# Kernel optimization log

Measured on AMD Instinct MI355X. Metric: run time of the kernel, lower is better.

Reference implementation:

```python
import jax, jax.numpy as jnp
import numpy as np

N = 100000      # nodes
E = 1600000     # edges (before self loops)
IN_DIM, EMB, HID, OUT, L = 128, 128, 128, 64, 3
LN_EPS = 1e-5


def _lin(k, fi, fo):
    return (jax.random.normal(k, (fi, fo), jnp.float32) / np.sqrt(fi)).astype(jnp.float32)


def setup_inputs() -> dict:
    key = jax.random.key(0)
    ks = jax.random.split(key, 8)
    x = jax.random.normal(ks[0], (N, IN_DIM), jnp.float32)
    edge_index = jax.random.randint(ks[1], (2, E), 0, N, dtype=jnp.int64)
    # in-degree of destination nodes (as data.degree would provide)
    degree = jnp.zeros((N,), jnp.float32).at[edge_index[1]].add(1.0)
    lks = jax.random.split(ks[2], 2 * L)
    W1 = jnp.stack([_lin(lks[2 * i], EMB, HID) for i in range(L)])
    W2 = jnp.stack([_lin(lks[2 * i + 1], HID, EMB) for i in range(L)])
    return dict(
        x=x, edge_index=edge_index, degree=degree,
        Win=_lin(ks[3], IN_DIM, EMB), b_in=jnp.zeros((EMB,), jnp.float32),
        W1=W1, b1=jnp.zeros((L, HID), jnp.float32),
        W2=W2, b2=jnp.zeros((L, EMB), jnp.float32),
        ln_g=jnp.ones((L, EMB), jnp.float32), ln_b=jnp.zeros((L, EMB), jnp.float32),
        out_g=jnp.ones((EMB,), jnp.float32), out_b=jnp.zeros((EMB,), jnp.float32),
        Wout=_lin(ks[4], EMB, OUT), b_out=jnp.zeros((OUT,), jnp.float32),
    )


def _layernorm(h, g, b):
    m = h.mean(-1, keepdims=True)
    v = ((h - m) ** 2).mean(-1, keepdims=True)
    return (h - m) * jax.lax.rsqrt(v + LN_EPS) * g + b


def reference(x, edge_index, degree, Win, b_in, W1, b1, W2, b2,
              ln_g, ln_b, out_g, out_b, Wout, b_out):
    # input_lin: Linear -> Dropout(eval: identity) -> ReLU
    h = jax.nn.relu(x @ Win + b_in)                        # [N, EMB]
    # add self loops, degree + 1
    loop = jnp.arange(N, dtype=edge_index.dtype)
    src = jnp.concatenate([edge_index[0], loop])           # [E+N]
    dst = jnp.concatenate([edge_index[1], loop])
    inv = jax.lax.rsqrt(degree + 1.0)                      # deg^{-1/2}
    coef = (inv[src] * inv[dst])[:, None]                  # symmetric GCN norm
    for i in range(L):
        m = h @ W1[i] + b1[i]                              # [N, HID]
        agg = jax.ops.segment_sum(m[src] * coef, dst, num_segments=N)  # gather-scatter
        out = agg @ W2[i] + b2[i]                          # [N, EMB]
        h = jax.nn.relu(_layernorm(out + h, ln_g[i], ln_b[i]))  # residual + LN + act (dropout=id)
    h = _layernorm(h, out_g, out_b)
    return h @ Wout + b_out
```

## Files before the change

kernel.cpp:

```cpp
#include <hip/hip_runtime.h>
#include <cstdint>
#include <cstddef>

typedef unsigned short u16;
typedef unsigned int u32;
typedef __attribute__((ext_vector_type(2))) unsigned short u16x2;
typedef __attribute__((ext_vector_type(4))) unsigned short u16x4;
typedef __attribute__((ext_vector_type(8))) unsigned short u16x8;
typedef __attribute__((ext_vector_type(8))) __bf16 bf16x8;
typedef __attribute__((ext_vector_type(4))) float f32x4;

#define PREP_F32   0
#define PREP_BF16  1
#define PREP_LN    2
#define EPI_IN    0
#define EPI_SCALE 1
#define EPI_NONE  3

__device__ __forceinline__ float wred(float v) {
#pragma unroll
  for (int m = 32; m >= 1; m >>= 1) v += __shfl_xor(v, m, 64);
  return v;
}
__device__ __forceinline__ u16 f2bf(float f) {
  u32 u = __float_as_uint(f);
  u += 0x7fffu + ((u >> 16) & 1u);
  return (u16)(u >> 16);
}
__device__ __forceinline__ float bflo(u32 u) { return __uint_as_float(u << 16); }
__device__ __forceinline__ float bfhi(u32 u) { return __uint_as_float(u & 0xffff0000u); }
__device__ __forceinline__ u32 pack2(float a, float b) {
  u32 ua = __float_as_uint(a); ua += 0x7fffu + ((ua >> 16) & 1u);
  u32 ub = __float_as_uint(b); ub += 0x7fffu + ((ub >> 16) & 1u);
  return (ua >> 16) | (ub & 0xffff0000u);
}

__global__ void scan_block_k(const float* __restrict__ deg, int* __restrict__ offs,
                             int* __restrict__ bsum, int N) {
  __shared__ int sh[256];
  int tid = threadIdx.x;
  int i = blockIdx.x * 256 + tid;
  int c = (i < N) ? (int)(deg[i] + 0.5f) : 0;
  int val = c;
  for (int off = 1; off < 256; off <<= 1) {
    sh[tid] = val; __syncthreads();
    if (tid >= off) val += sh[tid - off];
    __syncthreads();
  }
  if (i < N) offs[i] = val - c;
  if (tid == 255) bsum[blockIdx.x] = val;
}

__global__ void scan_bsum_k(int* __restrict__ bsum, int nb) {
  __shared__ int sh[1024];
  int tid = threadIdx.x;
  int c = (tid < nb) ? bsum[tid] : 0;
  int val = c;
  for (int off = 1; off < 1024; off <<= 1) {
    sh[tid] = val; __syncthreads();
    if (tid >= off) val += sh[tid - off];
    __syncthreads();
  }
  if (tid < nb) bsum[tid] = val - c;
}

__global__ void scan_add_k(int* __restrict__ offs, const int* __restrict__ bsum,
                           int* __restrict__ gcur, float* __restrict__ inv,
                           const float* __restrict__ deg, int N, int E) {
  int i = blockIdx.x * 256 + threadIdx.x;
  if (i < N) {
    int o = offs[i] + bsum[i >> 8];
    offs[i] = o;
    inv[i] = rsqrtf(deg[i] + 1.0f);
    if ((i & 511) == 0) gcur[i >> 9] = o;
  } else if (i == N) {
    offs[N] = E;
  }
}

__global__ __launch_bounds__(256) void scatter_k(
    const int* __restrict__ src, const int* __restrict__ dst,
    int* __restrict__ gcur, uint2* __restrict__ pairs, int E) {
  __shared__ int hist[256];
  __shared__ int base_[256];
  const int tid = threadIdx.x;
  const int e0 = blockIdx.x * 8192;
  const int e1 = min(E, e0 + 8192);
  hist[tid] = 0;
  __syncthreads();
  for (int e = e0 + tid; e < e1; e += 256)
    atomicAdd(&hist[dst[e] >> 9], 1);
  __syncthreads();
  int c = hist[tid];
  if (c > 0) base_[tid] = atomicAdd(&gcur[tid], c);
  hist[tid] = 0;
  __syncthreads();
  for (int e = e0 + tid; e < e1; e += 256) {
    int d = dst[e];
    int b = d >> 9;
    int r = atomicAdd(&hist[b], 1);
    pairs[base_[b] + r] = make_uint2((u32)src[e], (u32)d);
  }
}

__global__ __launch_bounds__(256) void fill2_k(
    const uint2* __restrict__ pairs, const int* __restrict__ offs,
    int* __restrict__ col, int N) {
  __shared__ int cur[512];
  const int b = blockIdx.x;
  const int n0 = b << 9;
  const int n1 = min(N, n0 + 512);
  const int tid = threadIdx.x;
  for (int i = tid; i < n1 - n0; i += 256) cur[i] = offs[n0 + i];
  __syncthreads();
  const int e0 = offs[n0], e1 = offs[n1];
  for (int e = e0 + tid; e < e1; e += 256) {
    uint2 pr = pairs[e];
    int p = atomicAdd(&cur[(int)pr.y - n0], 1);
    col[p] = (int)pr.x;
  }
}

__global__ void pack_all_k(const float* __restrict__ Win, const float* __restrict__ W1,
                           const float* __restrict__ W2, const float* __restrict__ Wout,
                           u16* __restrict__ pWin, u16* __restrict__ pW1,
                           u16* __restrict__ pW2, u16* __restrict__ pWout) {
  const int b = blockIdx.x;
  const float* W; u16* P; int ncol; int t;
  if (b < 8)       { W = Win;                        P = pWin;                      ncol = 128; t = b * 256 + threadIdx.x; }
  else if (b < 32) { int l = (b - 8) / 8;  W = W1 + (size_t)l * 16384;  P = pW1 + (size_t)l * 16384; ncol = 128; t = ((b - 8) % 8) * 256 + threadIdx.x; }
  else if (b < 56) { int l = (b - 32) / 8; W = W2 + (size_t)l * 16384;  P = pW2 + (size_t)l * 16384; ncol = 128; t = ((b - 32) % 8) * 256 + threadIdx.x; }
  else             { W = Wout;                       P = pWout;                     ncol = 64;  t = (b - 56) * 256 + threadIdx.x; }
  int NT = ncol >> 4;
  int total = 4 * NT * 64;
  if (t >= total) return;
  int lane = t & 63;
  int tmp = t >> 6;
  int nt = tmp % NT, kc = tmp / NT;
  int n = nt * 16 + (lane & 15);
  int kb = kc * 32 + ((lane >> 4) << 2);
  u16* dst = P + (size_t)t * 8;
#pragma unroll
  for (int j = 0; j < 8; ++j) {
    int k = kb + (j & 3) + ((j >> 2) << 4);
    dst[j] = f2bf(W[(size_t)k * ncol + n]);
  }
}

__global__ __launch_bounds__(256) void spmm_gemm_k(
    const uint4* __restrict__ msc, const int* __restrict__ offs,
    const int* __restrict__ col, const float* __restrict__ inv,
    const u16* __restrict__ Wp, const float* __restrict__ bias,
    u32* __restrict__ h, const float* __restrict__ g1,
    const float* __restrict__ lb1, int N) {
  __shared__ union {
    u16  xs[32][136];
    float cs[32][132];
  } sh;
  const int tid = threadIdx.x;
  const int lane = tid & 63, wid = tid >> 6;
  const int row0 = blockIdx.x * 32;
  const int g = lane >> 4, c = lane & 15;

  for (int rr = 0; rr < 8; ++rr) {
    const int d = row0 + wid * 8 + rr;
    const int s0 = offs[d], s1 = offs[d + 1];
    float2 a0 = {0.f, 0.f}, a1 = {0.f, 0.f}, a2 = {0.f, 0.f}, a3 = {0.f, 0.f};
    int base = s0;
    const int nfull = s0 + ((s1 - s0) & ~15);
    for (; base < nfull; base += 16) {
      int sA = col[base + g];
      int sB = col[base + 4 + g];
      int sC = col[base + 8 + g];
      int sD = col[base + 12 + g];
      uint4 rA = msc[(size_t)sA * 16 + c];
      uint4 rB = msc[(size_t)sB * 16 + c];
      uint4 rC = msc[(size_t)sC * 16 + c];
      uint4 rD = msc[(size_t)sD * 16 + c];
      a0.x += bflo(rA.x); a0.y += bfhi(rA.x);
      a1.x += bflo(rA.y); a1.y += bfhi(rA.y);
      a2.x += bflo(rA.z); a2.y += bfhi(rA.z);
      a3.x += bflo(rA.w); a3.y += bfhi(rA.w);
      a0.x += bflo(rB.x); a0.y += bfhi(rB.x);
      a1.x += bflo(rB.y); a1.y += bfhi(rB.y);
      a2.x += bflo(rB.z); a2.y += bfhi(rB.z);
      a3.x += bflo(rB.w); a3.y += bfhi(rB.w);
      a0.x += bflo(rC.x); a0.y += bfhi(rC.x);
      a1.x += bflo(rC.y); a1.y += bfhi(rC.y);
      a2.x += bflo(rC.z); a2.y += bfhi(rC.z);
      a3.x += bflo(rC.w); a3.y += bfhi(rC.w);
      a0.x += bflo(rD.x); a0.y += bfhi(rD.x);
      a1.x += bflo(rD.y); a1.y += bfhi(rD.y);
      a2.x += bflo(rD.z); a2.y += bfhi(rD.z);
      a3.x += bflo(rD.w); a3.y += bfhi(rD.w);
    }
    if (base < s1) {
      const int last = s1 - 1;
      int jA = base + g, jB = base + 4 + g, jC = base + 8 + g, jD = base + 12 + g;
      int sA = col[min(jA, last)];
      int sB = col[min(jB, last)];
      int sC = col[min(jC, last)];
      int sD = col[min(jD, last)];
      uint4 rA = msc[(size_t)sA * 16 + c];
      uint4 rB = msc[(size_t)sB * 16 + c];
      uint4 rC = msc[(size_t)sC * 16 + c];
      uint4 rD = msc[(size_t)sD * 16 + c];
      float mA = (jA <= last) ? 1.f : 0.f;
      float mB = (jB <= last) ? 1.f : 0.f;
      float mC = (jC <= last) ? 1.f : 0.f;
      float mD = (jD <= last) ? 1.f : 0.f;
      a0.x = fmaf(mA, bflo(rA.x), a0.x); a0.y = fmaf(mA, bfhi(rA.x), a0.y);
      a1.x = fmaf(mA, bflo(rA.y), a1.x); a1.y = fmaf(mA, bfhi(rA.y), a1.y);
      a2.x = fmaf(mA, bflo(rA.z), a2.x); a2.y = fmaf(mA, bfhi(rA.z), a2.y);
      a3.x = fmaf(mA, bflo(rA.w), a3.x); a3.y = fmaf(mA, bfhi(rA.w), a3.y);
      a0.x = fmaf(mB, bflo(rB.x), a0.x); a0.y = fmaf(mB, bfhi(rB.x), a0.y);
      a1.x = fmaf(mB, bflo(rB.y), a1.x); a1.y = fmaf(mB, bfhi(rB.y), a1.y);
      a2.x = fmaf(mB, bflo(rB.z), a2.x); a2.y = fmaf(mB, bfhi(rB.z), a2.y);
      a3.x = fmaf(mB, bflo(rB.w), a3.x); a3.y = fmaf(mB, bfhi(rB.w), a3.y);
      a0.x = fmaf(mC, bflo(rC.x), a0.x); a0.y = fmaf(mC, bfhi(rC.x), a0.y);
      a1.x = fmaf(mC, bflo(rC.y), a1.x); a1.y = fmaf(mC, bfhi(rC.y), a1.y);
      a2.x = fmaf(mC, bflo(rC.z), a2.x); a2.y = fmaf(mC, bfhi(rC.z), a2.y);
      a3.x = fmaf(mC, bflo(rC.w), a3.x); a3.y = fmaf(mC, bfhi(rC.w), a3.y);
      a0.x = fmaf(mD, bflo(rD.x), a0.x); a0.y = fmaf(mD, bfhi(rD.x), a0.y);
      a1.x = fmaf(mD, bflo(rD.y), a1.x); a1.y = fmaf(mD, bfhi(rD.y), a1.y);
      a2.x = fmaf(mD, bflo(rD.z), a2.x); a2.y = fmaf(mD, bfhi(rD.z), a2.y);
      a3.x = fmaf(mD, bflo(rD.w), a3.x); a3.y = fmaf(mD, bfhi(rD.w), a3.y);
    }
    a0.x += __shfl_xor(a0.x, 16, 64); a0.x += __shfl_xor(a0.x, 32, 64);
    a0.y += __shfl_xor(a0.y, 16, 64); a0.y += __shfl_xor(a0.y, 32, 64);
    a1.x += __shfl_xor(a1.x, 16, 64); a1.x += __shfl_xor(a1.x, 32, 64);
    a1.y += __shfl_xor(a1.y, 16, 64); a1.y += __shfl_xor(a1.y, 32, 64);
    a2.x += __shfl_xor(a2.x, 16, 64); a2.x += __shfl_xor(a2.x, 32, 64);
    a2.y += __shfl_xor(a2.y, 16, 64); a2.y += __shfl_xor(a2.y, 32, 64);
    a3.x += __shfl_xor(a3.x, 16, 64); a3.x += __shfl_xor(a3.x, 32, 64);
    a3.y += __shfl_xor(a3.y, 16, 64); a3.y += __shfl_xor(a3.y, 32, 64);
    if (g == 0) {
      uint4 r = msc[(size_t)d * 16 + c];
      float iv = inv[d];
      uint4 o;
      o.x = pack2((a0.x + bflo(r.x)) * iv, (a0.y + bfhi(r.x)) * iv);
      o.y = pack2((a1.x + bflo(r.y)) * iv, (a1.y + bfhi(r.y)) * iv);
      o.z = pack2((a2.x + bflo(r.z)) * iv, (a2.y + bfhi(r.z)) * iv);
      o.w = pack2((a3.x + bflo(r.w)) * iv, (a3.y + bfhi(r.w)) * iv);
      *(uint4*)&sh.xs[wid * 8 + rr][c * 8] = o;
    }
  }
  __syncthreads();

  const int m0  = (wid >> 1) << 4;
  const int ntb = (wid & 1) << 2;
  f32x4 acc[4];
#pragma unroll
  for (int t = 0; t < 4; ++t) acc[t] = (f32x4){0.f, 0.f, 0.f, 0.f};
  const int ar  = m0 + (lane & 15);
  const int akb = (lane >> 4) << 2;
  const bf16x8* Bp = (const bf16x8*)Wp;
#pragma unroll
  for (int kc = 0; kc < 4; ++kc) {
    u16x4 lo = *(const u16x4*)&sh.xs[ar][kc * 32 + akb];
    u16x4 hi = *(const u16x4*)&sh.xs[ar][kc * 32 + akb + 16];
    u16x8 av;
#pragma unroll
    for (int j = 0; j < 4; ++j) { av[j] = lo[j]; av[j + 4] = hi[j]; }
    bf16x8 a = __builtin_bit_cast(bf16x8, av);
#pragma unroll
    for (int t = 0; t < 4; ++t) {
      bf16x8 b = Bp[(kc * 8 + ntb + t) * 64 + lane];
      acc[t] = __builtin_amdgcn_mfma_f32_16x16x32_bf16(a, b, acc[t], 0, 0, 0);
    }
  }

  const int cb = lane & 15;
  const int rg = (lane >> 4) << 2;
  __syncthreads();
#pragma unroll
  for (int t = 0; t < 4; ++t) {
    int colm = (ntb + t) * 16 + cb;
    float bv = bias[colm];
#pragma unroll
    for (int r = 0; r < 4; ++r) sh.cs[m0 + rg + r][colm] = acc[t][r] + bv;
  }
  __syncthreads();
  float2 gg = *(const float2*)&g1[lane * 2];
  float2 bb = *(const float2*)&lb1[lane * 2];
  for (int rr = 0; rr < 8; ++rr) {
    int r = wid * 8 + rr;
    int gr = row0 + r;
    float2 t2 = *(const float2*)&sh.cs[r][lane * 2];
    u32 hv = h[(size_t)gr * 64 + lane];
    float tx = t2.x + bflo(hv), ty = t2.y + bfhi(hv);
    float mean = wred(tx + ty) * (1.f / 128.f);
    float dx = tx - mean, dy = ty - mean;
    float var = wred(dx * dx + dy * dy) * (1.f / 128.f);
    float rstd = rsqrtf(var + 1e-5f);
    float y0 = fmaxf(dx * rstd * gg.x + bb.x, 0.f);
    float y1 = fmaxf(dy * rstd * gg.y + bb.y, 0.f);
    h[(size_t)gr * 64 + lane] = pack2(y0, y1);
  }
}

template <int NOUT, int PREP, int EPI>
__global__ __launch_bounds__(256) void gemm_mfma(
    const void* __restrict__ Xv, const u16* __restrict__ Wp,
    const float* __restrict__ bias, void* __restrict__ Yv,
    const void* __restrict__ resv,
    const float* __restrict__ g1, const float* __restrict__ lb1,
    int N) {
  constexpr int NT = NOUT / 16;
  __shared__ union {
    u16  xs[32][136];
    float cs[32][132];
  } sh;
  const int tid = threadIdx.x;
  const int lane = tid & 63, wid = tid >> 6;
  const int row0 = blockIdx.x * 32;

  if constexpr (PREP == PREP_F32) {
    const float* X = (const float*)Xv;
    for (int i = tid; i < 1024; i += 256) {
      int r = i >> 5, c4 = i & 31;
      float4 v = ((const float4*)(X + (size_t)(row0 + r) * 128))[c4];
      u16x4 o = {f2bf(v.x), f2bf(v.y), f2bf(v.z), f2bf(v.w)};
      *(u16x4*)&sh.xs[r][c4 * 4] = o;
    }
  } else if constexpr (PREP == PREP_BF16) {
    const u16x4* X = (const u16x4*)Xv;
    for (int i = tid; i < 1024; i += 256) {
      int r = i >> 5, c4 = i & 31;
      *(u16x4*)&sh.xs[r][c4 * 4] = X[(size_t)(row0 + r) * 32 + c4];
    }
  } else {
    const u32* X = (const u32*)Xv;
    float2 gg = *(const float2*)&g1[lane * 2];
    float2 bb = *(const float2*)&lb1[lane * 2];
    for (int rr = 0; rr < 8; ++rr) {
      int r = wid * 8 + rr;
      u32 v = X[(size_t)(row0 + r) * 64 + lane];
      float tx = bflo(v), ty = bfhi(v);
      float mean = wred(tx + ty) * (1.f / 128.f);
      float dx = tx - mean, dy = ty - mean;
      float var = wred(dx * dx + dy * dy) * (1.f / 128.f);
      float rstd = rsqrtf(var + 1e-5f);
      u16x2 o = {f2bf(dx * rstd * gg.x + bb.x), f2bf(dy * rstd * gg.y + bb.y)};
      *(u16x2*)&sh.xs[r][lane * 2] = o;
    }
  }
  __syncthreads();

  constexpr int NTW = (NOUT == 128) ? 4 : 2;
  const int m0  = (NOUT == 128) ? ((wid >> 1) << 4) : ((wid & 1) << 4);
  const int ntb = (NOUT == 128) ? ((wid & 1) << 2) : ((wid >> 1) << 1);

  f32x4 acc[NTW];
#pragma unroll
  for (int t = 0; t < NTW; ++t) acc[t] = (f32x4){0.f, 0.f, 0.f, 0.f};

  const int ar  = m0 + (lane & 15);
  const int akb = (lane >> 4) << 2;
  const bf16x8* Bp = (const bf16x8*)Wp;
#pragma unroll
  for (int kc = 0; kc < 4; ++kc) {
    u16x4 lo = *(const u16x4*)&sh.xs[ar][kc * 32 + akb];
    u16x4 hi = *(const u16x4*)&sh.xs[ar][kc * 32 + akb + 16];
    u16x8 av;
#pragma unroll
    for (int j = 0; j < 4; ++j) { av[j] = lo[j]; av[j + 4] = hi[j]; }
    bf16x8 a = __builtin_bit_cast(bf16x8, av);
#pragma unroll
    for (int t = 0; t < NTW; ++t) {
      bf16x8 b = Bp[(kc * NT + ntb + t) * 64 + lane];
      acc[t] = __builtin_amdgcn_mfma_f32_16x16x32_bf16(a, b, acc[t], 0, 0, 0);
    }
  }

  const int cb = lane & 15;
  const int rg = (lane >> 4) << 2;
  if constexpr (EPI == EPI_NONE) {
    float* Y = (float*)Yv;
#pragma unroll
    for (int t = 0; t < NTW; ++t) {
      int col = (ntb + t) * 16 + cb;
      float bv = bias[col];
#pragma unroll
      for (int r = 0; r < 4; ++r) {
        int gr = row0 + m0 + rg + r;
        Y[(size_t)gr * NOUT + col] = acc[t][r] + bv;
      }
    }
  } else if constexpr (EPI == EPI_SCALE) {
    const float* inv = (const float*)resv;
    u16* Y = (u16*)Yv;
#pragma unroll
    for (int t = 0; t < NTW; ++t) {
      int col = (ntb + t) * 16 + cb;
      float bv = bias[col];
#pragma unroll
      for (int r = 0; r < 4; ++r) {
        int gr = row0 + m0 + rg + r;
        Y[(size_t)gr * NOUT + col] = f2bf((acc[t][r] + bv) * inv[gr]);
      }
    }
  } else {
    __syncthreads();
#pragma unroll
    for (int t = 0; t < NTW; ++t) {
      int col = (ntb + t) * 16 + cb;
      float bv = bias[col];
#pragma unroll
      for (int r = 0; r < 4; ++r) sh.cs[m0 + rg + r][col] = acc[t][r] + bv;
    }
    __syncthreads();
    u32* Y = (u32*)Yv;
    for (int rr = 0; rr < 8; ++rr) {
      int r = wid * 8 + rr;
      int gr = row0 + r;
      float2 t2 = *(const float2*)&sh.cs[r][lane * 2];
      Y[(size_t)gr * 64 + lane] = pack2(fmaxf(t2.x, 0.f), fmaxf(t2.y, 0.f));
    }
  }
}

extern "C" void kernel_launch(void* const* d_in, const int* in_sizes, int n_in,
                              void* d_out, int out_size, void* d_ws, size_t ws_size,
                              hipStream_t stream) {
  (void)n_in; (void)out_size; (void)ws_size;
  const float* x      = (const float*)d_in[0];
  const int*   eidx   = (const int*)d_in[1];
  const float* degree = (const float*)d_in[2];
  const float* Win    = (const float*)d_in[3];
  const float* b_in   = (const float*)d_in[4];
  const float* W1     = (const float*)d_in[5];
  const float* b1     = (const float*)d_in[6];
  const float* W2     = (const float*)d_in[7];
  const float* b2     = (const float*)d_in[8];
  const float* ln_g   = (const float*)d_in[9];
  const float* ln_b   = (const float*)d_in[10];
  const float* out_g  = (const float*)d_in[11];
  const float* out_b  = (const float*)d_in[12];
  const float* Wout   = (const float*)d_in[13];
  const float* b_out  = (const float*)d_in[14];

  const int N = in_sizes[0] / 128;
  const int E = in_sizes[1] / 2;
  const int* esrc = eidx;
  const int* edst = eidx + E;

  char* p = (char*)d_ws;
  auto alloc = [&](size_t bytes) {
    char* q = p;
    p += (bytes + 255) & ~(size_t)255;
    return q;
  };
  float* inv    = (float*)alloc((size_t)N * 4);
  int*   offs   = (int*)alloc(((size_t)N + 1) * 4);
  int*   gcur   = (int*)alloc(256 * 4);
  int*   bsum   = (int*)alloc(1024 * 4);
  int*   col    = (int*)alloc((size_t)E * 4);
  uint2* pairs  = (uint2*)alloc((size_t)E * 8);
  u32*   h      = (u32*)alloc((size_t)N * 128 * 2);
  u32*   msc    = (u32*)alloc((size_t)N * 128 * 2);
  u16*   pWin   = (u16*)alloc(4 * 8 * 64 * 8 * 2);
  u16*   pWout  = (u16*)alloc(4 * 4 * 64 * 8 * 2);
  u16*   pW1    = (u16*)alloc(3 * 4 * 8 * 64 * 8 * 2);
  u16*   pW2    = (u16*)alloc(3 * 4 * 8 * 64 * 8 * 2);

  pack_all_k<<<60, 256, 0, stream>>>(Win, W1, W2, Wout, pWin, pW1, pW2, pWout);

  const int nb = (N + 255) / 256;
  const int NB = (N + 511) / 512;
  scan_block_k<<<nb, 256, 0, stream>>>(degree, offs, bsum, N);
  scan_bsum_k<<<1, 1024, 0, stream>>>(bsum, nb);
  scan_add_k<<<(N + 256) / 256, 256, 0, stream>>>(offs, bsum, gcur, inv, degree, N, E);
  scatter_k<<<(E + 8191) / 8192, 256, 0, stream>>>(esrc, edst, gcur, pairs, E);
  fill2_k<<<NB, 256, 0, stream>>>(pairs, offs, col, N);

  const int gemmGrid = (N + 31) / 32;

  gemm_mfma<128, PREP_F32, EPI_IN><<<gemmGrid, 256, 0, stream>>>(
      x, pWin, b_in, h, nullptr, nullptr, nullptr, N);
  for (int l = 0; l < 3; ++l) {
    gemm_mfma<128, PREP_BF16, EPI_SCALE><<<gemmGrid, 256, 0, stream>>>(
        h, pW1 + (size_t)l * 16384, b1 + l * 128, msc, inv, nullptr, nullptr, N);
    spmm_gemm_k<<<gemmGrid, 256, 0, stream>>>(
        (const uint4*)msc, offs, col, inv, pW2 + (size_t)l * 16384,
        b2 + l * 128, h, ln_g + l * 128, ln_b + l * 128, N);
  }
  gemm_mfma<64, PREP_LN, EPI_NONE><<<gemmGrid, 256, 0, stream>>>(
      h, pWout, b_out, d_out, nullptr, out_g, out_b, N);
}
```

Baseline: 391.3 us.

## Pack edge pairs into 32 bits and map one row per quarter-wave in SpMM

The bucketed scatter now stores each edge as a single 32-bit word, holding the 17-bit source and the 9-bit local destination, which halves the pairs buffer traffic. In the fused SpMM+GEMM kernel each 16-lane group now owns its own destination row instead of the whole wave splitting one row's edges and reducing with cross-lane shuffles, which removes the shuffle reduction. Each group walks its neighbour list serially in steps of four with masking. The LayerNorm epilogue is split into two 16-row halves so the shared float buffer shrinks, at the cost of extra barriers. Packing assumes N < 131072, and per-row work imbalance within a wave may rise.

```diff
diff --git a/kernel.cpp b/kernel.cpp
--- a/kernel.cpp
+++ b/kernel.cpp
@@ -80,7 +80,7 @@
 
 __global__ __launch_bounds__(256) void scatter_k(
     const int* __restrict__ src, const int* __restrict__ dst,
-    int* __restrict__ gcur, uint2* __restrict__ pairs, int E) {
+    int* __restrict__ gcur, u32* __restrict__ pairs, int E) {
   __shared__ int hist[256];
   __shared__ int base_[256];
   const int tid = threadIdx.x;
@@ -99,12 +99,12 @@
     int d = dst[e];
     int b = d >> 9;
     int r = atomicAdd(&hist[b], 1);
-    pairs[base_[b] + r] = make_uint2((u32)src[e], (u32)d);
+    pairs[base_[b] + r] = (u32)src[e] | ((u32)(d & 511) << 17);
   }
 }
 
 __global__ __launch_bounds__(256) void fill2_k(
-    const uint2* __restrict__ pairs, const int* __restrict__ offs,
+    const u32* __restrict__ pairs, const int* __restrict__ offs,
     int* __restrict__ col, int N) {
   __shared__ int cur[512];
   const int b = blockIdx.x;
@@ -115,9 +115,9 @@
   __syncthreads();
   const int e0 = offs[n0], e1 = offs[n1];
   for (int e = e0 + tid; e < e1; e += 256) {
-    uint2 pr = pairs[e];
-    int p = atomicAdd(&cur[(int)pr.y - n0], 1);
-    col[p] = (int)pr.x;
+    u32 pr = pairs[e];
+    int p = atomicAdd(&cur[pr >> 17], 1);
+    col[p] = (int)(pr & 0x1FFFFu);
   }
 }
 
@@ -155,64 +155,36 @@
     const float* __restrict__ lb1, int N) {
   __shared__ union {
     u16  xs[32][136];
-    float cs[32][132];
+    float cs[16][132];
   } sh;
   const int tid = threadIdx.x;
   const int lane = tid & 63, wid = tid >> 6;
   const int row0 = blockIdx.x * 32;
-  const int g = lane >> 4, c = lane & 15;
-
-  for (int rr = 0; rr < 8; ++rr) {
-    const int d = row0 + wid * 8 + rr;
+  const int rgrp = lane >> 4, c = lane & 15;
+
+#pragma unroll
+  for (int p = 0; p < 2; ++p) {
+    const int lrow = wid * 8 + p * 4 + rgrp;
+    const int d = row0 + lrow;
     const int s0 = offs[d], s1 = offs[d + 1];
+    const int last = s1 - 1;
     float2 a0 = {0.f, 0.f}, a1 = {0.f, 0.f}, a2 = {0.f, 0.f}, a3 = {0.f, 0.f};
-    int base = s0;
-    const int nfull = s0 + ((s1 - s0) & ~15);
-    for (; base < nfull; base += 16) {
-      int sA = col[base + g];
-      int sB = col[base + 4 + g];
-      int sC = col[base + 8 + g];
-      int sD = col[base + 12 + g];
+    for (int k = s0; k < s1; k += 4) {
+      int sA = col[k];
+      int sB = col[min(k + 1, last)];
+      int sC = col[min(k + 2, last)];
+      int sD = col[min(k + 3, last)];
       uint4 rA = msc[(size_t)sA * 16 + c];
       uint4 rB = msc[(size_t)sB * 16 + c];
       uint4 rC = msc[(size_t)sC * 16 + c];
       uint4 rD = msc[(size_t)sD * 16 + c];
+      float mB = (k + 1 < s1) ? 1.f : 0.f;
+      float mC = (k + 2 < s1) ? 1.f : 0.f;
+      float mD = (k + 3 < s1) ? 1.f : 0.f;
       a0.x += bflo(rA.x); a0.y += bfhi(rA.x);
       a1.x += bflo(rA.y); a1.y += bfhi(rA.y);
       a2.x += bflo(rA.z); a2.y += bfhi(rA.z);
       a3.x += bflo(rA.w); a3.y += bfhi(rA.w);
-      a0.x += bflo(rB.x); a0.y += bfhi(rB.x);
-      a1.x += bflo(rB.y); a1.y += bfhi(rB.y);
-      a2.x += bflo(rB.z); a2.y += bfhi(rB.z);
-      a3.x += bflo(rB.w); a3.y += bfhi(rB.w);
-      a0.x += bflo(rC.x); a0.y += bfhi(rC.x);
-      a1.x += bflo(rC.y); a1.y += bfhi(rC.y);
-      a2.x += bflo(rC.z); a2.y += bfhi(rC.z);
-      a3.x += bflo(rC.w); a3.y += bfhi(rC.w);
-      a0.x += bflo(rD.x); a0.y += bfhi(rD.x);
-      a1.x += bflo(rD.y); a1.y += bfhi(rD.y);
-      a2.x += bflo(rD.z); a2.y += bfhi(rD.z);
-      a3.x += bflo(rD.w); a3.y += bfhi(rD.w);
-    }
-    if (base < s1) {
-      const int last = s1 - 1;
-      int jA = base + g, jB = base + 4 + g, jC = base + 8 + g, jD = base + 12 + g;
-      int sA = col[min(jA, last)];
-      int sB = col[min(jB, last)];
-      int sC = col[min(jC, last)];
-      int sD = col[min(jD, last)];
-      uint4 rA = msc[(size_t)sA * 16 + c];
-      uint4 rB = msc[(size_t)sB * 16 + c];
-      uint4 rC = msc[(size_t)sC * 16 + c];
-      uint4 rD = msc[(size_t)sD * 16 + c];
-      float mA = (jA <= last) ? 1.f : 0.f;
-      float mB = (jB <= last) ? 1.f : 0.f;
-      float mC = (jC <= last) ? 1.f : 0.f;
-      float mD = (jD <= last) ? 1.f : 0.f;
-      a0.x = fmaf(mA, bflo(rA.x), a0.x); a0.y = fmaf(mA, bfhi(rA.x), a0.y);
-      a1.x = fmaf(mA, bflo(rA.y), a1.x); a1.y = fmaf(mA, bfhi(rA.y), a1.y);
-      a2.x = fmaf(mA, bflo(rA.z), a2.x); a2.y = fmaf(mA, bfhi(rA.z), a2.y);
-      a3.x = fmaf(mA, bflo(rA.w), a3.x); a3.y = fmaf(mA, bfhi(rA.w), a3.y);
       a0.x = fmaf(mB, bflo(rB.x), a0.x); a0.y = fmaf(mB, bfhi(rB.x), a0.y);
       a1.x = fmaf(mB, bflo(rB.y), a1.x); a1.y = fmaf(mB, bfhi(rB.y), a1.y);
       a2.x = fmaf(mB, bflo(rB.z), a2.x); a2.y = fmaf(mB, bfhi(rB.z), a2.y);
@@ -226,24 +198,14 @@
       a2.x = fmaf(mD, bflo(rD.z), a2.x); a2.y = fmaf(mD, bfhi(rD.z), a2.y);
       a3.x = fmaf(mD, bflo(rD.w), a3.x); a3.y = fmaf(mD, bfhi(rD.w), a3.y);
     }
-    a0.x += __shfl_xor(a0.x, 16, 64); a0.x += __shfl_xor(a0.x, 32, 64);
-    a0.y += __shfl_xor(a0.y, 16, 64); a0.y += __shfl_xor(a0.y, 32, 64);
-    a1.x += __shfl_xor(a1.x, 16, 64); a1.x += __shfl_xor(a1.x, 32, 64);
-    a1.y += __shfl_xor(a1.y, 16, 64); a1.y += __shfl_xor(a1.y, 32, 64);
-    a2.x += __shfl_xor(a2.x, 16, 64); a2.x += __shfl_xor(a2.x, 32, 64);
-    a2.y += __shfl_xor(a2.y, 16, 64); a2.y += __shfl_xor(a2.y, 32, 64);
-    a3.x += __shfl_xor(a3.x, 16, 64); a3.x += __shfl_xor(a3.x, 32, 64);
-    a3.y += __shfl_xor(a3.y, 16, 64); a3.y += __shfl_xor(a3.y, 32, 64);
-    if (g == 0) {
-      uint4 r = msc[(size_t)d * 16 + c];
-      float iv = inv[d];
-      uint4 o;
-      o.x = pack2((a0.x + bflo(r.x)) * iv, (a0.y + bfhi(r.x)) * iv);
-      o.y = pack2((a1.x + bflo(r.y)) * iv, (a1.y + bfhi(r.y)) * iv);
-      o.z = pack2((a2.x + bflo(r.z)) * iv, (a2.y + bfhi(r.z)) * iv);
-      o.w = pack2((a3.x + bflo(r.w)) * iv, (a3.y + bfhi(r.w)) * iv);
-      *(uint4*)&sh.xs[wid * 8 + rr][c * 8] = o;
-    }
+    uint4 r = msc[(size_t)d * 16 + c];
+    float iv = inv[d];
+    uint4 o;
+    o.x = pack2((a0.x + bflo(r.x)) * iv, (a0.y + bfhi(r.x)) * iv);
+    o.y = pack2((a1.x + bflo(r.y)) * iv, (a1.y + bfhi(r.y)) * iv);
+    o.z = pack2((a2.x + bflo(r.z)) * iv, (a2.y + bfhi(r.z)) * iv);
+    o.w = pack2((a3.x + bflo(r.w)) * iv, (a3.y + bfhi(r.w)) * iv);
+    *(uint4*)&sh.xs[lrow][c * 8] = o;
   }
   __syncthreads();
 
@@ -272,30 +234,35 @@
 
   const int cb = lane & 15;
   const int rg = (lane >> 4) << 2;
-  __syncthreads();
-#pragma unroll
-  for (int t = 0; t < 4; ++t) {
-    int colm = (ntb + t) * 16 + cb;
-    float bv = bias[colm];
-#pragma unroll
-    for (int r = 0; r < 4; ++r) sh.cs[m0 + rg + r][colm] = acc[t][r] + bv;
-  }
-  __syncthreads();
   float2 gg = *(const float2*)&g1[lane * 2];
   float2 bb = *(const float2*)&lb1[lane * 2];
-  for (int rr = 0; rr < 8; ++rr) {
-    int r = wid * 8 + rr;
-    int gr = row0 + r;
-    float2 t2 = *(const float2*)&sh.cs[r][lane * 2];
-    u32 hv = h[(size_t)gr * 64 + lane];
-    float tx = t2.x + bflo(hv), ty = t2.y + bfhi(hv);
-    float mean = wred(tx + ty) * (1.f / 128.f);
-    float dx = tx - mean, dy = ty - mean;
-    float var = wred(dx * dx + dy * dy) * (1.f / 128.f);
-    float rstd = rsqrtf(var + 1e-5f);
-    float y0 = fmaxf(dx * rstd * gg.x + bb.x, 0.f);
-    float y1 = fmaxf(dy * rstd * gg.y + bb.y, 0.f);
-    h[(size_t)gr * 64 + lane] = pack2(y0, y1);
+#pragma unroll
+  for (int hh = 0; hh < 2; ++hh) {
+    __syncthreads();
+    if ((m0 >> 4) == hh) {
+#pragma unroll
+      for (int t = 0; t < 4; ++t) {
+        int colm = (ntb + t) * 16 + cb;
+        float bv = bias[colm];
+#pragma unroll
+        for (int r = 0; r < 4; ++r) sh.cs[rg + r][colm] = acc[t][r] + bv;
+      }
+    }
+    __syncthreads();
+    for (int rr = 0; rr < 4; ++rr) {
+      int lr = wid * 4 + rr;
+      int gr = row0 + hh * 16 + lr;
+      float2 t2 = *(const float2*)&sh.cs[lr][lane * 2];
+      u32 hv = h[(size_t)gr * 64 + lane];
+      float tx = t2.x + bflo(hv), ty = t2.y + bfhi(hv);
+      float mean = wred(tx + ty) * (1.f / 128.f);
+      float dx = tx - mean, dy = ty - mean;
+      float var = wred(dx * dx + dy * dy) * (1.f / 128.f);
+      float rstd = rsqrtf(var + 1e-5f);
+      float y0 = fmaxf(dx * rstd * gg.x + bb.x, 0.f);
+      float y1 = fmaxf(dy * rstd * gg.y + bb.y, 0.f);
+      h[(size_t)gr * 64 + lane] = pack2(y0, y1);
+    }
   }
 }
 
@@ -456,7 +423,7 @@
   int*   gcur   = (int*)alloc(256 * 4);
   int*   bsum   = (int*)alloc(1024 * 4);
   int*   col    = (int*)alloc((size_t)E * 4);
-  uint2* pairs  = (uint2*)alloc((size_t)E * 8);
+  u32*   pairs  = (u32*)alloc((size_t)E * 4);
   u32*   h      = (u32*)alloc((size_t)N * 128 * 2);
   u32*   msc    = (u32*)alloc((size_t)N * 128 * 2);
   u16*   pWin   = (u16*)alloc(4 * 8 * 64 * 8 * 2);
```

Result: faster. 371.4 us (-5.1%).
